# Optimization experiments

Measured on AMD Instinct MI355X. Metric: run time of the kernel, lower is better.

## Reference

```python
import jax, jax.numpy as jnp
from jax import lax
import numpy as np

C_IN, H, W = 9, 11, 11
N_FILT = 64
N_LAYERS = 8
FC_UNITS = 64
LSTM_H = 64
N_ACTIONS = 6
B, T = 32, 128


def setup_inputs() -> dict:
    key = jax.random.key(0)
    ks = jax.random.split(key, 24)
    s = 0.05
    d = {}
    d['x'] = jax.random.normal(ks[0], (B, T, C_IN, H, W), dtype=jnp.float32)
    d['conv0_w'] = jax.random.normal(ks[1], (N_FILT, C_IN, 3, 3), dtype=jnp.float32) * s
    d['conv0_b'] = jnp.zeros((N_FILT,), jnp.float32)
    d['conv_ws'] = jax.random.normal(ks[2], (N_LAYERS - 1, N_FILT, N_FILT, 3, 3), dtype=jnp.float32) * s
    d['conv_bs'] = jnp.zeros((N_LAYERS - 1, N_FILT), jnp.float32)
    d['fc_w'] = jax.random.normal(ks[3], (FC_UNITS, N_FILT * H * W), dtype=jnp.float32) * s
    d['fc_b'] = jnp.zeros((FC_UNITS,), jnp.float32)
    d['w_ih'] = jax.random.normal(ks[4], (4 * LSTM_H, FC_UNITS), dtype=jnp.float32) * s
    d['w_hh'] = jax.random.normal(ks[5], (4 * LSTM_H, LSTM_H), dtype=jnp.float32) * s
    d['b_ih'] = jnp.zeros((4 * LSTM_H,), jnp.float32)
    d['b_hh'] = jnp.zeros((4 * LSTM_H,), jnp.float32)
    d['p1_w'] = jax.random.normal(ks[6], (128, LSTM_H), dtype=jnp.float32) * s
    d['p1_b'] = jnp.zeros((128,), jnp.float32)
    d['p2_w'] = jax.random.normal(ks[7], (N_ACTIONS, 128), dtype=jnp.float32) * s
    d['p2_b'] = jnp.zeros((N_ACTIONS,), jnp.float32)
    d['v1_w'] = jax.random.normal(ks[8], (128, LSTM_H), dtype=jnp.float32) * s
    d['v1_b'] = jnp.zeros((128,), jnp.float32)
    d['v2_w'] = jax.random.normal(ks[9], (1, 128), dtype=jnp.float32) * s
    d['v2_b'] = jnp.zeros((1,), jnp.float32)
    return d


def _conv_relu(h, w, b):
    # h: [N, C, H, W], w: [O, I, 3, 3] -> SAME padding, stride 1
    y = lax.conv_general_dilated(h, w, (1, 1), [(1, 1), (1, 1)],
                                 dimension_numbers=('NCHW', 'OIHW', 'NCHW'))
    return jax.nn.relu(y + b[None, :, None, None])


def _forward(x, conv0_w, conv0_b, conv_ws, conv_bs, fc_w, fc_b,
             w_ih, w_hh, b_ih, b_hh, p1_w, p1_b, p2_w, p2_b, v1_w, v1_b, v2_w, v2_b):
    b, t = x.shape[0], x.shape[1]
    h = x.reshape(b * t, C_IN, H, W)          # batch CNN over all frames at once
    h = _conv_relu(h, conv0_w, conv0_b)
    for i in range(N_LAYERS - 1):             # fixed small layer loop
        h = _conv_relu(h, conv_ws[i], conv_bs[i])
    h = h.reshape(b * t, N_FILT * H * W)
    feats = jax.nn.relu(h @ fc_w.T + fc_b)    # [B*T, FC_UNITS]
    feats = feats.reshape(b, t, FC_UNITS)

    # LSTM (PyTorch gate order i, f, g, o)
    def step(carry, xt):
        hprev, cprev = carry
        g = xt @ w_ih.T + hprev @ w_hh.T + b_ih + b_hh
        i_g, f_g, g_g, o_g = jnp.split(g, 4, axis=-1)
        c = jax.nn.sigmoid(f_g) * cprev + jax.nn.sigmoid(i_g) * jnp.tanh(g_g)
        hn = jax.nn.sigmoid(o_g) * jnp.tanh(c)
        return (hn, c), hn

    h0 = jnp.zeros((b, LSTM_H), feats.dtype)
    c0 = jnp.zeros((b, LSTM_H), feats.dtype)
    _, outs = lax.scan(step, (h0, c0), jnp.swapaxes(feats, 0, 1))  # [T, B, H]
    lstm_out = jnp.swapaxes(outs, 0, 1)       # [B, T, H]

    p = jax.nn.relu(lstm_out @ p1_w.T + p1_b) @ p2_w.T + p2_b  # [B, T, n_actions]
    v = jax.nn.relu(lstm_out @ v1_w.T + v1_b) @ v2_w.T + v2_b  # [B, T, 1]
    return p, v


def reference(x, conv0_w, conv0_b, conv_ws, conv_bs, fc_w, fc_b,
              w_ih, w_hh, b_ih, b_hh, p1_w, p1_b, p2_w, p2_b, v1_w, v1_b, v2_w, v2_b):
    return _forward(x, conv0_w, conv0_b, conv_ws, conv_bs, fc_w, fc_b,
                    w_ih, w_hh, b_ih, b_hh, p1_w, p1_b, p2_w, p2_b,
                    v1_w, v1_b, v2_w, v2_b)
```

## Files before the change

kernel.cpp:

```cpp
#include <hip/hip_runtime.h>
#include <hip/hip_bf16.h>

typedef __attribute__((ext_vector_type(8))) short short8;
typedef __attribute__((ext_vector_type(4))) short short4_t;
typedef __attribute__((ext_vector_type(4))) float floatx4;
typedef __attribute__((ext_vector_type(16))) float floatx16;

#define MFMA_B16(a,b,c) __builtin_amdgcn_mfma_f32_16x16x32_bf16((a),(b),(c),0,0,0)
#define MFMA32(a,b,c)   __builtin_amdgcn_mfma_f32_32x32x16_bf16((a),(b),(c),0,0,0)

__device__ __forceinline__ short f2bf(float f) {
    union { __hip_bfloat16 h; short s; } u;
    u.h = __float2bfloat16(f);
    return u.s;
}

union S8U { short4_t h[2]; short8 v; };

#define N_FRAMES 4096
#define C_IN     9
#define POS      121
#define NF       64
#define FC_K     7744
#define ISTR     20
#define FSZ      10816

#define OFF_W0    0
#define OFF_WP    18432
#define OFF_FCP   534528
#define OFF_WIHT  1525760
#define OFF_BSUM  1591296
#define OFF_ACTS  1592320
#define OFF_XG    66079744
#define OFF_HOUT  70274048

__global__ __launch_bounds__(256) void prep_kernel(
    const float* __restrict__ conv0_w, const float* __restrict__ conv_ws,
    const float* __restrict__ w_ih,
    const float* __restrict__ b_ih, const float* __restrict__ b_hh,
    short* __restrict__ w0, short* __restrict__ wpk,
    float* __restrict__ wihT, float* __restrict__ bsum)
{
    int idx = blockIdx.x*256 + threadIdx.x;
    if (idx < 9216) {
        int tap = idx >> 10; int r = idx & 1023;
        int mt = r >> 9; int o = (r >> 4) & 31; int ci = r & 15;
        int oc = mt*32 + o;
        float v = (ci < 9) ? conv0_w[(oc*9 + ci)*9 + tap] : 0.f;
        w0[idx] = f2bf(v);
        return;
    }
    idx -= 9216;
    if (idx < 258048) {
        int l = idx / 36864; int r = idx % 36864;
        int tap = r >> 12; int rr = r & 4095;
        int mt = rr >> 11;
        int ks = (rr >> 9) & 3;
        int o  = (rr >> 4) & 31;
        int ci16 = rr & 15;
        int oc = mt*32 + o;
        int ci = ks*16 + ci16;
        wpk[idx] = f2bf(conv_ws[((l*64 + oc)*64 + ci)*9 + tap]);
        return;
    }
    idx -= 258048;
    if (idx < 16384) {
        int k = idx >> 8; int g = idx & 255;
        wihT[idx] = w_ih[g*64 + k];
        return;
    }
    idx -= 16384;
    if (idx < 256) bsum[idx] = b_ih[idx] + b_hh[idx];
}

__global__ __launch_bounds__(256) void fc_transpose(
    const float* __restrict__ fc_w, short* __restrict__ fcp)
{
    __shared__ float row[FC_K];
    const int u = blockIdx.x;
    const int tid = threadIdx.x;
    const float* src = fc_w + (size_t)u*FC_K;
    for (int i = tid; i < FC_K; i += 256) row[i] = src[i];
    __syncthreads();
    short* dst = fcp + (size_t)u*FC_K;
    for (int k2 = tid; k2 < FC_K; k2 += 256) {
        int p = k2 >> 6, c = k2 & 63;
        dst[k2] = f2bf(row[c*121 + p]);
    }
}

__global__ __launch_bounds__(128, 3) void conv_stack(
    const float* __restrict__ x,
    const float* __restrict__ conv0_b,
    const float* __restrict__ conv_bs,
    const short* __restrict__ w0,
    const short* __restrict__ wpk,
    short* __restrict__ acts_out)
{
    __shared__ alignas(16) short act[FSZ];
    const int tid  = threadIdx.x;
    const int lane = tid & 63;
    const int wv   = tid >> 6;
    const int n    = lane & 31;
    const int kh   = lane >> 5;
    char* actb = (char*)act;

    const short8 zero8 = {0,0,0,0,0,0,0,0};
    const floatx16 fz16 = {};

    for (int i = tid*8; i < 3392; i += 1024) *(short8*)(&act[i]) = zero8;
    __syncthreads();

    {
        const float* xf = x + (size_t)blockIdx.x*(C_IN*POS);
        for (int i = tid; i < C_IN*POS; i += 128) {
            int ci = i / POS;
            int p  = i - ci*POS;
            int yy = p / 11;
            int xx = p - yy*11;
            act[((yy+1)*13 + (xx+1))*ISTR + ci] = f2bf(xf[i]);
        }
    }
    __syncthreads();

    floatx16 acc[2][2];
    #pragma unroll
    for (int mt=0;mt<2;mt++)
        #pragma unroll
        for (int j=0;j<2;j++) acc[mt][j] = fz16;

    int cell20[2], vbase[2], wbase[2];
    #pragma unroll
    for (int j = 0; j < 2; ++j) {
        int p = (wv*2 + j)*32 + n;
        int pc = (p <= 120) ? p : 120;
        int yy = pc / 11, xx = pc - yy*11;
        int cell = yy*13 + xx;
        cell20[j] = cell*ISTR;
        vbase[j]  = cell*128;
        wbase[j]  = (cell + 14)*128;
    }
    const bool tail = (wv == 1) && (n > 24);

    {
        const short* w0l = w0 + n*16 + kh*8;
        #pragma unroll 1
        for (int dy = 0; dy < 3; ++dy) {
            #pragma unroll 1
            for (int dx = 0; dx < 3; ++dx) {
                const short* wt = w0l + (dy*3+dx)*1024;
                short8 a0 = *(const short8*)(wt);
                short8 a1 = *(const short8*)(wt + 512);
                const int so = (dy*13+dx)*ISTR + kh*8;
                #pragma unroll
                for (int j=0;j<2;j++) {
                    const short* bp = act + cell20[j] + so;
                    S8U t;
                    t.h[0] = *(const short4_t*)(bp);
                    t.h[1] = *(const short4_t*)(bp + 4);
                    acc[0][j] = MFMA32(a0, t.v, acc[0][j]);
                    acc[1][j] = MFMA32(a1, t.v, acc[1][j]);
                }
            }
        }
    }

    __syncthreads();
    for (int i = tid*8; i < FSZ; i += 1024) *(short8*)(&act[i]) = zero8;

    auto epilogue = [&](const float* bias) {
        __syncthreads();
        #pragma unroll
        for (int mt=0;mt<2;mt++) {
            #pragma unroll
            for (int q=0;q<4;q++) {
                const int ch0 = mt*32 + q*8 + kh*4;
                const floatx4 bb = *(const floatx4*)(bias + ch0);
                const int soff = (((mt*4 + q + n) & 7) << 4) + kh*8;
                #pragma unroll
                for (int j=0;j<2;j++) {
                    if (j == 1 && tail) continue;
                    short4_t sv;
                    sv.x = f2bf(fmaxf(acc[mt][j][q*4+0] + bb.x, 0.f));
                    sv.y = f2bf(fmaxf(acc[mt][j][q*4+1] + bb.y, 0.f));
                    sv.z = f2bf(fmaxf(acc[mt][j][q*4+2] + bb.z, 0.f));
                    sv.w = f2bf(fmaxf(acc[mt][j][q*4+3] + bb.w, 0.f));
                    *(short4_t*)(actb + wbase[j] + soff) = sv;
                }
            }
        }
        #pragma unroll
        for (int mt=0;mt<2;mt++)
            #pragma unroll
            for (int j=0;j<2;j++) acc[mt][j] = fz16;
        __syncthreads();
    };

    epilogue(conv0_b);

    {
        short8 AX0,AX1,AX2,AX3, AY0,AY1,AY2,AY3;
        #pragma unroll 1
        for (int l = 1; l < 8; ++l) {
            const short* wl = wpk + (l-1)*36864 + n*16 + kh*8;
            AX0 = *(const short8*)(wl);
            AX1 = *(const short8*)(wl + 2048);
            AX2 = *(const short8*)(wl + 512);
            AX3 = *(const short8*)(wl + 2560);
            #pragma unroll
            for (int i = 0; i < 18; ++i) {
                const int tp = i >> 1, kp = i & 1;
                const int sb_ = ((tp/3)*13 + (tp%3))*128;
                const int cu_ = (tp/3)*11 + (tp%3) + 4 + kh + n + 4*kp;
                const int so0 = sb_ + ((cu_ & 7) << 4);
                const int so1 = sb_ + (((cu_ + 2) & 7) << 4);
                short8 b00 = *(const short8*)(actb + vbase[0] + so0);
                short8 b01 = *(const short8*)(actb + vbase[1] + so0);
                short8 b10 = *(const short8*)(actb + vbase[0] + so1);
                short8 b11 = *(const short8*)(actb + vbase[1] + so1);
                if (i < 17) {
                    const int j = i + 1;
                    const short* wt_ = wl + (j>>1)*4096 + (j&1)*1024;
                    if ((i & 1) == 0) {
                        AY0 = *(const short8*)(wt_);
                        AY1 = *(const short8*)(wt_ + 2048);
                        AY2 = *(const short8*)(wt_ + 512);
                        AY3 = *(const short8*)(wt_ + 2560);
                    } else {
                        AX0 = *(const short8*)(wt_);
                        AX1 = *(const short8*)(wt_ + 2048);
                        AX2 = *(const short8*)(wt_ + 512);
                        AX3 = *(const short8*)(wt_ + 2560);
                    }
                }
                __builtin_amdgcn_sched_barrier(0);
                if ((i & 1) == 0) {
                    acc[0][0]=MFMA32(AX0,b00,acc[0][0]); acc[1][0]=MFMA32(AX1,b00,acc[1][0]);
                    acc[0][1]=MFMA32(AX0,b01,acc[0][1]); acc[1][1]=MFMA32(AX1,b01,acc[1][1]);
                    acc[0][0]=MFMA32(AX2,b10,acc[0][0]); acc[1][0]=MFMA32(AX3,b10,acc[1][0]);
                    acc[0][1]=MFMA32(AX2,b11,acc[0][1]); acc[1][1]=MFMA32(AX3,b11,acc[1][1]);
                } else {
                    acc[0][0]=MFMA32(AY0,b00,acc[0][0]); acc[1][0]=MFMA32(AY1,b00,acc[1][0]);
                    acc[0][1]=MFMA32(AY0,b01,acc[0][1]); acc[1][1]=MFMA32(AY1,b01,acc[1][1]);
                    acc[0][0]=MFMA32(AY2,b10,acc[0][0]); acc[1][0]=MFMA32(AY3,b10,acc[1][0]);
                    acc[0][1]=MFMA32(AY2,b11,acc[0][1]); acc[1][1]=MFMA32(AY3,b11,acc[1][1]);
                }
            }
            epilogue(conv_bs + (l-1)*NF);
        }
    }

    {
        short* dst = acts_out + (size_t)blockIdx.x*FC_K;
        #pragma unroll 1
        for (int it = 0; it < 8; ++it) {
            int q = it*128 + tid;
            if (q < 968) {
                int p = q >> 3, G = q & 7;
                int yy = p / 11, xx = p - yy*11;
                int cell = (yy+1)*13 + (xx+1);
                int slot = (G + p) & 7;
                short8 v = *(const short8*)(actb + cell*128 + slot*16);
                *(short8*)(dst + q*8) = v;
            }
        }
    }
}

__global__ __launch_bounds__(256) void fc_xg_kernel(
    const short* __restrict__ acts, const short* __restrict__ fcp,
    const float* __restrict__ fc_b, const float* __restrict__ wihT,
    const float* __restrict__ bsum, float* __restrict__ xg)
{
    __shared__ alignas(16) float red[3*64*16];
    __shared__ alignas(16) float fbuf[16*64];
    const int tid  = threadIdx.x;
    const int lane = tid & 63;
    const int w    = tid >> 6;
    const int m    = lane & 15;
    const int kg   = lane >> 4;
    const int bm   = blockIdx.x;

    const floatx4 fzero = {0.f,0.f,0.f,0.f};
    floatx4 acc[4];
    #pragma unroll
    for (int nt=0;nt<4;nt++) acc[nt] = fzero;

    const short* arow = acts + (size_t)(bm*16 + m)*FC_K + kg*8;
    const short* brow = fcp + (size_t)m*FC_K + kg*8;

    for (int kc = w; kc < 242; kc += 4) {
        short8 a = *(const short8*)(arow + kc*32);
        #pragma unroll
        for (int nt=0;nt<4;nt++) {
            short8 b = *(const short8*)(brow + (size_t)nt*16*FC_K + kc*32);
            acc[nt] = MFMA_B16(a, b, acc[nt]);
        }
    }

    if (w > 0) {
        #pragma unroll
        for (int nt=0;nt<4;nt++)
            *(floatx4*)(&red[((w-1)*64 + lane)*16 + nt*4]) = acc[nt];
    }
    __syncthreads();
    if (w == 0) {
        #pragma unroll
        for (int nt=0;nt<4;nt++)
            for (int j=0;j<3;j++)
                acc[nt] += *(const floatx4*)(&red[(j*64 + lane)*16 + nt*4]);
        #pragma unroll
        for (int nt=0;nt<4;nt++) {
            int unit = nt*16 + m;
            float bias = fc_b[unit];
            int fr = kg*4;
            fbuf[(fr+0)*NF + unit] = fmaxf(acc[nt].x + bias, 0.f);
            fbuf[(fr+1)*NF + unit] = fmaxf(acc[nt].y + bias, 0.f);
            fbuf[(fr+2)*NF + unit] = fmaxf(acc[nt].z + bias, 0.f);
            fbuf[(fr+3)*NF + unit] = fmaxf(acc[nt].w + bias, 0.f);
        }
    }
    __syncthreads();

    {
        const int g = tid;
        float a[16];
        float bs = bsum[g];
        #pragma unroll
        for (int i=0;i<16;i++) a[i] = bs;
        for (int k=0;k<64;k++) {
            float wk = wihT[k*256 + g];
            #pragma unroll
            for (int i=0;i<16;i++) a[i] += fbuf[i*64 + k] * wk;
        }
        float* xo = xg + (size_t)(bm*16)*256 + g;
        #pragma unroll
        for (int i=0;i<16;i++) xo[i*256] = a[i];
    }
}

__device__ __forceinline__ float sigmf_(float v){
    return __builtin_amdgcn_rcpf(1.f + __expf(-v));
}
__device__ __forceinline__ float tanhf_(float v){
    return 1.f - 2.f*__builtin_amdgcn_rcpf(__expf(2.f*v) + 1.f);
}

__global__ __launch_bounds__(128) void lstm_kernel(
    const float* __restrict__ xg, const float* __restrict__ whh,
    float* __restrict__ hout)
{
    __shared__ alignas(16) float hbuf[64];
    __shared__ alignas(16) float gbuf[256];
    const int t = threadIdx.x;
    const int b = blockIdx.x;

    float4 w0v[16], w1v[16];
    #pragma unroll
    for (int k=0;k<16;k++) w0v[k] = *(const float4*)(whh + t*64 + k*4);
    #pragma unroll
    for (int k=0;k<16;k++) w1v[k] = *(const float4*)(whh + (t+128)*64 + k*4);

    float c = 0.f;
    if (t < 64) hbuf[t] = 0.f;
    __syncthreads();

    const float* xr = xg + (size_t)(b*128)*256;
    float nA = xr[t];
    float nB = xr[t+128];

    for (int ts=0; ts<128; ++ts) {
        float aA = nA, aB = nB;
        if (ts + 1 < 128) {
            const float* xn = xr + (ts+1)*256;
            nA = xn[t];
            nB = xn[t+128];
        }
        #pragma unroll
        for (int k=0;k<16;k++) {
            float4 hv = *(const float4*)(&hbuf[k*4]);
            aA += hv.x*w0v[k].x + hv.y*w0v[k].y + hv.z*w0v[k].z + hv.w*w0v[k].w;
            aB += hv.x*w1v[k].x + hv.y*w1v[k].y + hv.z*w1v[k].z + hv.w*w1v[k].w;
        }
        gbuf[t] = aA;
        gbuf[t+128] = aB;
        __syncthreads();
        if (t < 64) {
            float ig = sigmf_(gbuf[t]);
            float fg = sigmf_(gbuf[64+t]);
            float gg = tanhf_(gbuf[128+t]);
            float og = sigmf_(gbuf[192+t]);
            c = fg*c + ig*gg;
            float h = og*tanhf_(c);
            hbuf[t] = h;
            hout[(b*128+ts)*64 + t] = h;
        }
        __syncthreads();
    }
}

__global__ __launch_bounds__(64) void heads_kernel(
    const float* __restrict__ hout,
    const float* __restrict__ p1w, const float* __restrict__ p1b,
    const float* __restrict__ p2w, const float* __restrict__ p2b,
    const float* __restrict__ v1w, const float* __restrict__ v1b,
    const float* __restrict__ v2w, const float* __restrict__ v2b,
    float* __restrict__ out)
{
    __shared__ alignas(16) float hbuf[64];
    __shared__ alignas(16) float a1[128];
    __shared__ alignas(16) float a2[128];
    const int lane = threadIdx.x;
    for (int fi=0; fi<4; ++fi) {
        const int f = blockIdx.x*4 + fi;
        hbuf[lane] = hout[f*64 + lane];
        __syncthreads();
        #pragma unroll
        for (int uu=0; uu<2; ++uu) {
            const int u = lane + uu*64;
            float s1 = p1b[u], s2 = v1b[u];
            const float4* wp1 = (const float4*)(p1w + u*64);
            const float4* wv1 = (const float4*)(v1w + u*64);
            #pragma unroll
            for (int k=0;k<16;k++) {
                float4 h4 = *(const float4*)(&hbuf[k*4]);
                float4 w4 = wp1[k];
                s1 += h4.x*w4.x + h4.y*w4.y + h4.z*w4.z + h4.w*w4.w;
                float4 q4 = wv1[k];
                s2 += h4.x*q4.x + h4.y*q4.y + h4.z*q4.z + h4.w*q4.w;
            }
            a1[u] = fmaxf(s1, 0.f);
            a2[u] = fmaxf(s2, 0.f);
        }
        __syncthreads();
        if (lane < 6) {
            float s = p2b[lane];
            const float* wr = p2w + lane*128;
            #pragma unroll
            for (int j=0;j<128;j++) s += a1[j]*wr[j];
            out[f*6 + lane] = s;
        }
        if (lane == 6) {
            float s = v2b[0];
            #pragma unroll
            for (int j=0;j<128;j++) s += a2[j]*v2w[j];
            out[24576 + f] = s;
        }
        __syncthreads();
    }
}

extern "C" void kernel_launch(void* const* d_in, const int* in_sizes, int n_in,
                              void* d_out, int out_size, void* d_ws, size_t ws_size,
                              hipStream_t stream) {
    const float* x       = (const float*)d_in[0];
    const float* conv0_w = (const float*)d_in[1];
    const float* conv0_b = (const float*)d_in[2];
    const float* conv_ws = (const float*)d_in[3];
    const float* conv_bs = (const float*)d_in[4];
    const float* fc_w    = (const float*)d_in[5];
    const float* fc_b    = (const float*)d_in[6];
    const float* w_ih    = (const float*)d_in[7];
    const float* w_hh    = (const float*)d_in[8];
    const float* b_ih    = (const float*)d_in[9];
    const float* b_hh    = (const float*)d_in[10];
    const float* p1_w    = (const float*)d_in[11];
    const float* p1_b    = (const float*)d_in[12];
    const float* p2_w    = (const float*)d_in[13];
    const float* p2_b    = (const float*)d_in[14];
    const float* v1_w    = (const float*)d_in[15];
    const float* v1_b    = (const float*)d_in[16];
    const float* v2_w    = (const float*)d_in[17];
    const float* v2_b    = (const float*)d_in[18];
    float* out = (float*)d_out;

    char* ws = (char*)d_ws;
    short* w0    = (short*)(ws + OFF_W0);
    short* wpk   = (short*)(ws + OFF_WP);
    short* fcp   = (short*)(ws + OFF_FCP);
    float* wihT  = (float*)(ws + OFF_WIHT);
    float* bsum  = (float*)(ws + OFF_BSUM);
    short* acts  = (short*)(ws + OFF_ACTS);
    float* xgb   = (float*)(ws + OFF_XG);
    float* hout  = (float*)(ws + OFF_HOUT);

    prep_kernel<<<1109, 256, 0, stream>>>(conv0_w, conv_ws, w_ih, b_ih, b_hh,
                                          w0, wpk, wihT, bsum);
    fc_transpose<<<64, 256, 0, stream>>>(fc_w, fcp);
    conv_stack<<<N_FRAMES, 128, 0, stream>>>(x, conv0_b, conv_bs, w0, wpk, acts);
    fc_xg_kernel<<<256, 256, 0, stream>>>(acts, fcp, fc_b, wihT, bsum, xgb);
    lstm_kernel<<<32, 128, 0, stream>>>(xgb, w_hh, hout);
    heads_kernel<<<1024, 64, 0, stream>>>(hout, p1_w, p1_b, p2_w, p2_b,
                                          v1_w, v1_b, v2_w, v2_b, out);
}
```

Before: 505.0 us.

## Merge fc transpose into prep, widen LSTM block, parallelize heads per frame

Folds the fc weight transpose into the prep kernel so there is one fewer launch. The LSTM kernel now uses 256 threads with one gate row per thread, and splits the dot product across four accumulators to shorten the dependency chain on the serial recurrence. The heads kernel now runs one block per frame instead of four frames per block, and spreads the second-layer dot products over 56 lanes with shuffle reductions instead of a serial 128-long loop in a handful of lanes. Register pressure changes and the extra LSTM wave per block add barrier cost.

```diff
diff --git a/kernel.cpp b/kernel.cpp
--- a/kernel.cpp
+++ b/kernel.cpp
@@ -38,10 +38,26 @@
     const float* __restrict__ conv0_w, const float* __restrict__ conv_ws,
     const float* __restrict__ w_ih,
     const float* __restrict__ b_ih, const float* __restrict__ b_hh,
+    const float* __restrict__ fc_w,
     short* __restrict__ w0, short* __restrict__ wpk,
-    float* __restrict__ wihT, float* __restrict__ bsum)
+    float* __restrict__ wihT, float* __restrict__ bsum,
+    short* __restrict__ fcp)
 {
-    int idx = blockIdx.x*256 + threadIdx.x;
+    __shared__ float row[FC_K];
+    const int tid = threadIdx.x;
+    if (blockIdx.x < 64) {
+        const int u = blockIdx.x;
+        const float* src = fc_w + (size_t)u*FC_K;
+        for (int i = tid; i < FC_K; i += 256) row[i] = src[i];
+        __syncthreads();
+        short* dst = fcp + (size_t)u*FC_K;
+        for (int k2 = tid; k2 < FC_K; k2 += 256) {
+            int p = k2 >> 6, c = k2 & 63;
+            dst[k2] = f2bf(row[c*121 + p]);
+        }
+        return;
+    }
+    int idx = (blockIdx.x - 64)*256 + tid;
     if (idx < 9216) {
         int tap = idx >> 10; int r = idx & 1023;
         int mt = r >> 9; int o = (r >> 4) & 31; int ci = r & 15;
@@ -71,22 +87,6 @@
     }
     idx -= 16384;
     if (idx < 256) bsum[idx] = b_ih[idx] + b_hh[idx];
-}
-
-__global__ __launch_bounds__(256) void fc_transpose(
-    const float* __restrict__ fc_w, short* __restrict__ fcp)
-{
-    __shared__ float row[FC_K];
-    const int u = blockIdx.x;
-    const int tid = threadIdx.x;
-    const float* src = fc_w + (size_t)u*FC_K;
-    for (int i = tid; i < FC_K; i += 256) row[i] = src[i];
-    __syncthreads();
-    short* dst = fcp + (size_t)u*FC_K;
-    for (int k2 = tid; k2 < FC_K; k2 += 256) {
-        int p = k2 >> 6, c = k2 & 63;
-        dst[k2] = f2bf(row[c*121 + p]);
-    }
 }
 
 __global__ __launch_bounds__(128, 3) void conv_stack(
@@ -346,54 +346,52 @@
     return 1.f - 2.f*__builtin_amdgcn_rcpf(__expf(2.f*v) + 1.f);
 }
 
-__global__ __launch_bounds__(128) void lstm_kernel(
+__global__ __launch_bounds__(256) void lstm_kernel(
     const float* __restrict__ xg, const float* __restrict__ whh,
     float* __restrict__ hout)
 {
     __shared__ alignas(16) float hbuf[64];
     __shared__ alignas(16) float gbuf[256];
-    const int t = threadIdx.x;
+    const int g = threadIdx.x;
     const int b = blockIdx.x;
 
-    float4 w0v[16], w1v[16];
+    float4 wv[16];
     #pragma unroll
-    for (int k=0;k<16;k++) w0v[k] = *(const float4*)(whh + t*64 + k*4);
-    #pragma unroll
-    for (int k=0;k<16;k++) w1v[k] = *(const float4*)(whh + (t+128)*64 + k*4);
+    for (int k=0;k<16;k++) wv[k] = *(const float4*)(whh + g*64 + k*4);
 
     float c = 0.f;
-    if (t < 64) hbuf[t] = 0.f;
+    if (g < 64) hbuf[g] = 0.f;
     __syncthreads();
 
     const float* xr = xg + (size_t)(b*128)*256;
-    float nA = xr[t];
-    float nB = xr[t+128];
+    float nx = xr[g];
 
     for (int ts=0; ts<128; ++ts) {
-        float aA = nA, aB = nB;
-        if (ts + 1 < 128) {
-            const float* xn = xr + (ts+1)*256;
-            nA = xn[t];
-            nB = xn[t+128];
-        }
-        #pragma unroll
-        for (int k=0;k<16;k++) {
-            float4 hv = *(const float4*)(&hbuf[k*4]);
-            aA += hv.x*w0v[k].x + hv.y*w0v[k].y + hv.z*w0v[k].z + hv.w*w0v[k].w;
-            aB += hv.x*w1v[k].x + hv.y*w1v[k].y + hv.z*w1v[k].z + hv.w*w1v[k].w;
-        }
-        gbuf[t] = aA;
-        gbuf[t+128] = aB;
+        float a0 = nx, a1 = 0.f, a2 = 0.f, a3 = 0.f;
+        if (ts + 1 < 128) nx = xr[(ts+1)*256 + g];
+        #pragma unroll
+        for (int k=0;k<4;k++) {
+            float4 h0 = *(const float4*)(&hbuf[k*16]);
+            float4 h1 = *(const float4*)(&hbuf[k*16+4]);
+            float4 h2 = *(const float4*)(&hbuf[k*16+8]);
+            float4 h3 = *(const float4*)(&hbuf[k*16+12]);
+            float4 w0 = wv[k*4+0], w1 = wv[k*4+1], w2 = wv[k*4+2], w3 = wv[k*4+3];
+            a0 += h0.x*w0.x + h0.y*w0.y + h0.z*w0.z + h0.w*w0.w;
+            a1 += h1.x*w1.x + h1.y*w1.y + h1.z*w1.z + h1.w*w1.w;
+            a2 += h2.x*w2.x + h2.y*w2.y + h2.z*w2.z + h2.w*w2.w;
+            a3 += h3.x*w3.x + h3.y*w3.y + h3.z*w3.z + h3.w*w3.w;
+        }
+        gbuf[g] = (a0 + a1) + (a2 + a3);
         __syncthreads();
-        if (t < 64) {
-            float ig = sigmf_(gbuf[t]);
-            float fg = sigmf_(gbuf[64+t]);
-            float gg = tanhf_(gbuf[128+t]);
-            float og = sigmf_(gbuf[192+t]);
+        if (g < 64) {
+            float ig = sigmf_(gbuf[g]);
+            float fg = sigmf_(gbuf[64+g]);
+            float gg = tanhf_(gbuf[128+g]);
+            float og = sigmf_(gbuf[192+g]);
             c = fg*c + ig*gg;
             float h = og*tanhf_(c);
-            hbuf[t] = h;
-            hout[(b*128+ts)*64 + t] = h;
+            hbuf[g] = h;
+            hout[(b*128+ts)*64 + g] = h;
         }
         __syncthreads();
     }
@@ -407,46 +405,56 @@
     const float* __restrict__ v2w, const float* __restrict__ v2b,
     float* __restrict__ out)
 {
-    __shared__ alignas(16) float hbuf[64];
+    __shared__ alignas(16) float hbv[64];
     __shared__ alignas(16) float a1[128];
     __shared__ alignas(16) float a2[128];
     const int lane = threadIdx.x;
-    for (int fi=0; fi<4; ++fi) {
-        const int f = blockIdx.x*4 + fi;
-        hbuf[lane] = hout[f*64 + lane];
-        __syncthreads();
-        #pragma unroll
-        for (int uu=0; uu<2; ++uu) {
-            const int u = lane + uu*64;
-            float s1 = p1b[u], s2 = v1b[u];
-            const float4* wp1 = (const float4*)(p1w + u*64);
-            const float4* wv1 = (const float4*)(v1w + u*64);
-            #pragma unroll
-            for (int k=0;k<16;k++) {
-                float4 h4 = *(const float4*)(&hbuf[k*4]);
-                float4 w4 = wp1[k];
-                s1 += h4.x*w4.x + h4.y*w4.y + h4.z*w4.z + h4.w*w4.w;
-                float4 q4 = wv1[k];
-                s2 += h4.x*q4.x + h4.y*q4.y + h4.z*q4.z + h4.w*q4.w;
-            }
-            a1[u] = fmaxf(s1, 0.f);
-            a2[u] = fmaxf(s2, 0.f);
-        }
-        __syncthreads();
-        if (lane < 6) {
-            float s = p2b[lane];
-            const float* wr = p2w + lane*128;
-            #pragma unroll
-            for (int j=0;j<128;j++) s += a1[j]*wr[j];
-            out[f*6 + lane] = s;
-        }
-        if (lane == 6) {
-            float s = v2b[0];
-            #pragma unroll
-            for (int j=0;j<128;j++) s += a2[j]*v2w[j];
-            out[24576 + f] = s;
-        }
-        __syncthreads();
+    const int f = blockIdx.x;
+    hbv[lane] = hout[f*64 + lane];
+    __syncthreads();
+    #pragma unroll
+    for (int uu=0; uu<2; ++uu) {
+        const int u = lane + uu*64;
+        const float4* wp1 = (const float4*)(p1w + u*64);
+        const float4* wv1 = (const float4*)(v1w + u*64);
+        float s1a=0.f,s1b=0.f,s1c=0.f,s1d=0.f;
+        float s2a=0.f,s2b=0.f,s2c=0.f,s2d=0.f;
+        #pragma unroll
+        for (int k=0;k<4;k++) {
+            float4 h0 = *(const float4*)(&hbv[k*16]);
+            float4 h1 = *(const float4*)(&hbv[k*16+4]);
+            float4 h2 = *(const float4*)(&hbv[k*16+8]);
+            float4 h3 = *(const float4*)(&hbv[k*16+12]);
+            float4 w0 = wp1[k*4+0], w1 = wp1[k*4+1], w2 = wp1[k*4+2], w3 = wp1[k*4+3];
+            s1a += h0.x*w0.x + h0.y*w0.y + h0.z*w0.z + h0.w*w0.w;
+            s1b += h1.x*w1.x + h1.y*w1.y + h1.z*w1.z + h1.w*w1.w;
+            s1c += h2.x*w2.x + h2.y*w2.y + h2.z*w2.z + h2.w*w2.w;
+            s1d += h3.x*w3.x + h3.y*w3.y + h3.z*w3.z + h3.w*w3.w;
+            float4 q0 = wv1[k*4+0], q1 = wv1[k*4+1], q2 = wv1[k*4+2], q3 = wv1[k*4+3];
+            s2a += h0.x*q0.x + h0.y*q0.y + h0.z*q0.z + h0.w*q0.w;
+            s2b += h1.x*q1.x + h1.y*q1.y + h1.z*q1.z + h1.w*q1.w;
+            s2c += h2.x*q2.x + h2.y*q2.y + h2.z*q2.z + h2.w*q2.w;
+            s2d += h3.x*q3.x + h3.y*q3.y + h3.z*q3.z + h3.w*q3.w;
+        }
+        a1[u] = fmaxf(p1b[u] + (s1a+s1b)+(s1c+s1d), 0.f);
+        a2[u] = fmaxf(v1b[u] + (s2a+s2b)+(s2c+s2d), 0.f);
+    }
+    __syncthreads();
+    if (lane < 56) {
+        const int o = lane >> 3, part = lane & 7;
+        const float* src = (o < 6) ? a1 : a2;
+        const float* wr  = (o < 6) ? (p2w + o*128) : v2w;
+        float s = 0.f;
+        const int j0 = part*16;
+        #pragma unroll
+        for (int j=0;j<16;j++) s += src[j0+j]*wr[j0+j];
+        s += __shfl_xor(s, 1);
+        s += __shfl_xor(s, 2);
+        s += __shfl_xor(s, 4);
+        if (part == 0) {
+            if (o < 6) out[f*6 + o] = p2b[o] + s;
+            else       out[24576 + f] = v2b[0] + s;
+        }
     }
 }
 
@@ -484,12 +492,11 @@
     float* xgb   = (float*)(ws + OFF_XG);
     float* hout  = (float*)(ws + OFF_HOUT);
 
-    prep_kernel<<<1109, 256, 0, stream>>>(conv0_w, conv_ws, w_ih, b_ih, b_hh,
-                                          w0, wpk, wihT, bsum);
-    fc_transpose<<<64, 256, 0, stream>>>(fc_w, fcp);
+    prep_kernel<<<1173, 256, 0, stream>>>(conv0_w, conv_ws, w_ih, b_ih, b_hh,
+                                          fc_w, w0, wpk, wihT, bsum, fcp);
     conv_stack<<<N_FRAMES, 128, 0, stream>>>(x, conv0_b, conv_bs, w0, wpk, acts);
     fc_xg_kernel<<<256, 256, 0, stream>>>(acts, fcp, fc_b, wihT, bsum, xgb);
-    lstm_kernel<<<32, 128, 0, stream>>>(xgb, w_hh, hout);
-    heads_kernel<<<1024, 64, 0, stream>>>(hout, p1_w, p1_b, p2_w, p2_b,
+    lstm_kernel<<<32, 256, 0, stream>>>(xgb, w_hh, hout);
+    heads_kernel<<<4096, 64, 0, stream>>>(hout, p1_w, p1_b, p2_w, p2_b,
                                           v1_w, v1_b, v2_w, v2_b, out);
 }
```

New measurement: 500.8 us. About the same (-0.8%).
